# Performance work log

Measured on AMD Instinct MI355X. Metric: run time of the kernel, lower is better.

The kernel has to match this reference:

```python
import jax, jax.numpy as jnp
import numpy as np

TRANSLATE_STD = 0.125
SCALE_STD = 0.2
CUTOUT_SIZE = 0.5

B, C, H, W = 64, 3, 512, 512


def setup_inputs() -> dict:
    key = jax.random.key(0)
    ks = jax.random.split(key, 20)
    inp = {
        'images': jax.random.normal(ks[0], (B, C, H, W), dtype=jnp.float32),
        'u_angle': jax.random.uniform(ks[1], (B,), dtype=jnp.float32),
        'u_scale': jax.random.uniform(ks[2], (B,), dtype=jnp.float32),
        'u_trans': jax.random.uniform(ks[3], (B,), dtype=jnp.float32),
        'u_bright': jax.random.uniform(ks[4], (B,), dtype=jnp.float32),
        'u_contrast': jax.random.uniform(ks[5], (B,), dtype=jnp.float32),
        'u_sat': jax.random.uniform(ks[6], (B,), dtype=jnp.float32),
        'noise': jax.random.normal(ks[7], (B, C, H, W), dtype=jnp.float32),
        'm_flip': jax.random.randint(ks[8], (B,), 0, 2, dtype=jnp.int32),
        'm_rot': jax.random.randint(ks[9], (B,), 0, 2, dtype=jnp.int32),
        'm_scale': jax.random.randint(ks[10], (B,), 0, 2, dtype=jnp.int32),
        'm_trans': jax.random.randint(ks[11], (B,), 0, 2, dtype=jnp.int32),
        'm_bright': jax.random.randint(ks[12], (B,), 0, 2, dtype=jnp.int32),
        'm_contrast': jax.random.randint(ks[13], (B,), 0, 2, dtype=jnp.int32),
        'm_sat': jax.random.randint(ks[14], (B,), 0, 2, dtype=jnp.int32),
        'm_cut': jax.random.randint(ks[15], (B,), 0, 2, dtype=jnp.int32),
        'y0': jax.random.randint(ks[16], (B,), 0, H - int(H * CUTOUT_SIZE) + 1, dtype=jnp.int32),
        'x0': jax.random.randint(ks[17], (B,), 0, W - int(W * CUTOUT_SIZE) + 1, dtype=jnp.int32),
    }
    return inp


def _sample_bilinear_reflect(img, gx, gy):
    # img: [C,H,W]; gx, gy: [H,W] normalized coords in grid_sample convention
    # (align_corners=False, padding_mode='reflection')
    c, h, w = img.shape
    x = ((gx + 1.0) * w - 1.0) * 0.5
    y = ((gy + 1.0) * h - 1.0) * 0.5

    def reflect(v, size):
        # reflect about pixel edges [-0.5, size-0.5], then clip coordinate
        v = jnp.abs(v + 0.5)
        v = jnp.mod(v, 2.0 * size)
        v = jnp.minimum(v, 2.0 * size - v)
        return jnp.clip(v - 0.5, 0.0, size - 1.0)

    x = reflect(x, float(w))
    y = reflect(y, float(h))
    x0f = jnp.floor(x)
    y0f = jnp.floor(y)
    wx = x - x0f
    wy = y - y0f
    x0i = jnp.clip(x0f, 0, w - 1).astype(jnp.int32)
    x1i = jnp.clip(x0f + 1, 0, w - 1).astype(jnp.int32)
    y0i = jnp.clip(y0f, 0, h - 1).astype(jnp.int32)
    y1i = jnp.clip(y0f + 1, 0, h - 1).astype(jnp.int32)
    v00 = img[:, y0i, x0i]
    v01 = img[:, y0i, x1i]
    v10 = img[:, y1i, x0i]
    v11 = img[:, y1i, x1i]
    top = v00 + wx * (v01 - v00)
    bot = v10 + wx * (v11 - v10)
    return top + wy * (bot - top)


def reference(images, u_angle, u_scale, u_trans, u_bright, u_contrast, u_sat,
              noise, m_flip, m_rot, m_scale, m_trans, m_bright, m_contrast,
              m_sat, m_cut, y0, x0):
    b, c, h, w = images.shape
    # xflip
    images = jnp.where((m_flip > 0)[:, None, None, None], images[..., ::-1], images)
    # rotate / scale / translate (single value broadcast to both axes, as in original)
    angle = jnp.where(m_rot > 0, (u_angle * 2.0 - 1.0) * jnp.pi, 0.0)
    sc = jnp.where(m_scale > 0, (u_scale * 2.0 - 1.0) * SCALE_STD + 1.0, 1.0)
    tr = jnp.where(m_trans > 0, (u_trans * 2.0 - 1.0) * TRANSLATE_STD, 0.0)
    ca = jnp.cos(angle)[:, None, None]
    sa = jnp.sin(angle)[:, None, None]
    scb = sc[:, None, None]
    trb = tr[:, None, None]
    gx0, gy0 = jnp.meshgrid(jnp.linspace(-1.0, 1.0, w), jnp.linspace(-1.0, 1.0, h), indexing='xy')  # [H,W]
    gx = scb * (ca * gx0 - sa * gy0) + trb  # [B,H,W]
    gy = scb * (sa * gx0 + ca * gy0) + trb
    images = jax.vmap(_sample_bilinear_reflect)(images, gx, gy)
    # brightness
    bb = jnp.where(m_bright > 0, u_bright * 0.2, 0.0)
    images = jnp.clip(images + bb[:, None, None, None], -1.0, 1.0)
    # contrast
    cc = jnp.where(m_contrast > 0, u_contrast + 0.5, 1.0)
    images = jnp.clip(images * cc[:, None, None, None], -1.0, 1.0)
    # saturation: lerp(grayscale, images, s)
    ss = jnp.where(m_sat > 0, u_sat * 2.0, 1.0)[:, None, None, None]
    gray = images.mean(axis=1, keepdims=True)
    images = jnp.clip(gray + ss * (images - gray), -1.0, 1.0)
    ch, cw = int(h * CUTOUT_SIZE), int(w * CUTOUT_SIZE)
    ys = jnp.arange(h)[None, :, None]
    xs = jnp.arange(w)[None, None, :]
    y0b = y0[:, None, None]
    x0b = x0[:, None, None]
    cmask = (ys >= y0b) & (ys < y0b + ch) & (xs >= x0b) & (xs < x0b + cw)
    fmask = cmask & (m_cut > 0)[:, None, None]
    images = jnp.where(fmask[:, None, :, :], noise, images)
    return images
```

## Files before the change

### kernel.cpp

```cpp
#include <hip/hip_runtime.h>
#include <math.h>


constexpr int Bn = 64;
constexpr int Cn = 3;
constexpr int Hn = 512;
constexpr int Wn = 512;
constexpr float TRANSLATE_STD = 0.125f;
constexpr float SCALE_STD = 0.2f;
constexpr int CUT_H = 256;
constexpr int CUT_W = 256;

typedef float f2v __attribute__((ext_vector_type(2)));

__device__ __forceinline__ f2v load2(const float* p) {
    f2v r;
    __builtin_memcpy(&r, p, 8);
    return r;
}

__device__ __forceinline__ float reflect_coord(float v, float size) {
    v = fabsf(v + 0.5f);
    v = fmodf(v, 2.0f * size);
    v = fminf(v, 2.0f * size - v);
    return fminf(fmaxf(v - 0.5f, 0.0f), size - 1.0f);
}

__global__ __launch_bounds__(256) void augment_kernel(
    const float* __restrict__ images,
    const float* __restrict__ u_angle,
    const float* __restrict__ u_scale,
    const float* __restrict__ u_trans,
    const float* __restrict__ u_bright,
    const float* __restrict__ u_contrast,
    const float* __restrict__ u_sat,
    const float* __restrict__ noise,
    const int* __restrict__ m_flip,
    const int* __restrict__ m_rot,
    const int* __restrict__ m_scale,
    const int* __restrict__ m_trans,
    const int* __restrict__ m_bright,
    const int* __restrict__ m_contrast,
    const int* __restrict__ m_sat,
    const int* __restrict__ m_cut,
    const int* __restrict__ y0p,
    const int* __restrict__ x0p,
    float* __restrict__ out)
{
    const int x = blockIdx.x * 32 + threadIdx.x;
    const int y = blockIdx.y * 8 + threadIdx.y;
    const int b = blockIdx.z;

    const float angle = (m_rot[b] > 0) ? (u_angle[b] * 2.0f - 1.0f) * 3.14159265358979323846f : 0.0f;
    const float sc    = (m_scale[b] > 0) ? (u_scale[b] * 2.0f - 1.0f) * SCALE_STD + 1.0f : 1.0f;
    const float tr    = (m_trans[b] > 0) ? (u_trans[b] * 2.0f - 1.0f) * TRANSLATE_STD : 0.0f;
    const float bb    = (m_bright[b] > 0) ? u_bright[b] * 0.2f : 0.0f;
    const float cc    = (m_contrast[b] > 0) ? u_contrast[b] + 0.5f : 1.0f;
    const float ss    = (m_sat[b] > 0) ? u_sat[b] * 2.0f : 1.0f;
    const bool  flip  = m_flip[b] > 0;
    const bool  docut = m_cut[b] > 0;
    const int   cy0   = y0p[b];
    const int   cx0   = x0p[b];

    float saf, caf;
    __sincosf(angle, &saf, &caf);

    const float gx0 = -1.0f + (2.0f / 511.0f) * (float)x;
    const float gy0 = -1.0f + (2.0f / 511.0f) * (float)y;

    const float gx = sc * (caf * gx0 - saf * gy0) + tr;
    const float gy = sc * (saf * gx0 + caf * gy0) + tr;

    float xx = ((gx + 1.0f) * (float)Wn - 1.0f) * 0.5f;
    float yy = ((gy + 1.0f) * (float)Hn - 1.0f) * 0.5f;
    xx = reflect_coord(xx, (float)Wn);
    yy = reflect_coord(yy, (float)Hn);

    const float x0f = floorf(xx);
    const float y0f = floorf(yy);
    const float wx = xx - x0f;
    const float wy = yy - y0f;

    int x0i = (int)fminf(fmaxf(x0f, 0.0f), (float)(Wn - 1));
    int x1i = (int)fminf(x0f + 1.0f, (float)(Wn - 1));
    const int y0i = (int)fminf(fmaxf(y0f, 0.0f), (float)(Hn - 1));
    const int y1i = (int)fminf(y0f + 1.0f, (float)(Hn - 1));

    if (flip) { x0i = (Wn - 1) - x0i; x1i = (Wn - 1) - x1i; }

    const int xbase = min(min(x0i, x1i), Wn - 2);
    const bool s0 = (x0i != xbase);
    const bool s1 = (x1i != xbase);

    const size_t plane = (size_t)Hn * Wn;
    const float* imgb = images + (size_t)b * Cn * plane;
    const int r0 = y0i * Wn + xbase;
    const int r1 = y1i * Wn + xbase;

    float vals[Cn];
    #pragma unroll
    for (int c = 0; c < Cn; ++c) {
        const float* p = imgb + (size_t)c * plane;
        const f2v t0 = load2(p + r0);
        const f2v t1 = load2(p + r1);
        const float v00 = s0 ? t0.y : t0.x;
        const float v01 = s1 ? t0.y : t0.x;
        const float v10 = s0 ? t1.y : t1.x;
        const float v11 = s1 ? t1.y : t1.x;
        const float top = v00 + wx * (v01 - v00);
        const float bot = v10 + wx * (v11 - v10);
        float v = top + wy * (bot - top);
        v = fminf(fmaxf(v + bb, -1.0f), 1.0f);
        v = fminf(fmaxf(v * cc, -1.0f), 1.0f);
        vals[c] = v;
    }

    const float gray = (vals[0] + vals[1] + vals[2]) * (1.0f / 3.0f);
    const bool cut = docut && (y >= cy0) && (y < cy0 + CUT_H) && (x >= cx0) && (x < cx0 + CUT_W);

    const size_t base = (size_t)b * Cn * plane + (size_t)y * Wn + (size_t)x;
    #pragma unroll
    for (int c = 0; c < Cn; ++c) {
        float v = gray + ss * (vals[c] - gray);
        v = fminf(fmaxf(v, -1.0f), 1.0f);
        if (cut) v = __builtin_nontemporal_load(&noise[base + c * plane]);
        __builtin_nontemporal_store(v, &out[base + c * plane]);
    }
}

extern "C" void kernel_launch(void* const* d_in, const int* in_sizes, int n_in,
                              void* d_out, int out_size, void* d_ws, size_t ws_size,
                              hipStream_t stream) {
    const float* images     = (const float*)d_in[0];
    const float* u_angle    = (const float*)d_in[1];
    const float* u_scale    = (const float*)d_in[2];
    const float* u_trans    = (const float*)d_in[3];
    const float* u_bright   = (const float*)d_in[4];
    const float* u_contrast = (const float*)d_in[5];
    const float* u_sat      = (const float*)d_in[6];
    const float* noise      = (const float*)d_in[7];
    const int*   m_flip     = (const int*)d_in[8];
    const int*   m_rot      = (const int*)d_in[9];
    const int*   m_scale    = (const int*)d_in[10];
    const int*   m_trans    = (const int*)d_in[11];
    const int*   m_bright   = (const int*)d_in[12];
    const int*   m_contrast = (const int*)d_in[13];
    const int*   m_sat      = (const int*)d_in[14];
    const int*   m_cut      = (const int*)d_in[15];
    const int*   y0p        = (const int*)d_in[16];
    const int*   x0p        = (const int*)d_in[17];
    float* out = (float*)d_out;

    dim3 block(32, 8);
    dim3 grid(Wn / 32, Hn / 8, Bn);
    augment_kernel<<<grid, block, 0, stream>>>(
        images, u_angle, u_scale, u_trans, u_bright, u_contrast, u_sat, noise,
        m_flip, m_rot, m_scale, m_trans, m_bright, m_contrast, m_sat, m_cut,
        y0p, x0p, out);
}
```

Measured before the change: 511.4 us.

## Stage source footprint of each tile in LDS for bilinear gather

Each 32x8 block works out the bounding box its tile maps to in the source image by transforming the tile's four corners. When that box lies inside the image and fits in the LDS capacity, the block cooperatively copies the footprint for all three channels into shared memory, with flip applied. It then does the bilinear sampling from LDS instead of issuing scattered global gathers. Blocks whose footprint needs reflection or is too large fall back to the original global-gather path, and the staged path adds a __syncthreads plus about 15KB of LDS per block.

```diff
diff --git a/kernel.cpp b/kernel.cpp
--- a/kernel.cpp
+++ b/kernel.cpp
@@ -10,6 +10,8 @@
 constexpr float SCALE_STD = 0.2f;
 constexpr int CUT_H = 256;
 constexpr int CUT_W = 256;
+
+constexpr int LDS_CAP = 1280;
 
 typedef float f2v __attribute__((ext_vector_type(2)));
 
@@ -47,6 +49,8 @@
     const int* __restrict__ x0p,
     float* __restrict__ out)
 {
+    __shared__ float lds[Cn * LDS_CAP];
+
     const int x = blockIdx.x * 32 + threadIdx.x;
     const int y = blockIdx.y * 8 + threadIdx.y;
     const int b = blockIdx.z;
@@ -65,54 +69,141 @@
     float saf, caf;
     __sincosf(angle, &saf, &caf);
 
-    const float gx0 = -1.0f + (2.0f / 511.0f) * (float)x;
-    const float gy0 = -1.0f + (2.0f / 511.0f) * (float)y;
-
-    const float gx = sc * (caf * gx0 - saf * gy0) + tr;
-    const float gy = sc * (saf * gx0 + caf * gy0) + tr;
-
-    float xx = ((gx + 1.0f) * (float)Wn - 1.0f) * 0.5f;
-    float yy = ((gy + 1.0f) * (float)Hn - 1.0f) * 0.5f;
-    xx = reflect_coord(xx, (float)Wn);
-    yy = reflect_coord(yy, (float)Hn);
-
-    const float x0f = floorf(xx);
-    const float y0f = floorf(yy);
-    const float wx = xx - x0f;
-    const float wy = yy - y0f;
-
-    int x0i = (int)fminf(fmaxf(x0f, 0.0f), (float)(Wn - 1));
-    int x1i = (int)fminf(x0f + 1.0f, (float)(Wn - 1));
-    const int y0i = (int)fminf(fmaxf(y0f, 0.0f), (float)(Hn - 1));
-    const int y1i = (int)fminf(y0f + 1.0f, (float)(Hn - 1));
-
-    if (flip) { x0i = (Wn - 1) - x0i; x1i = (Wn - 1) - x1i; }
-
-    const int xbase = min(min(x0i, x1i), Wn - 2);
-    const bool s0 = (x0i != xbase);
-    const bool s1 = (x1i != xbase);
+    auto coord = [&](float fx, float fy, float& oxx, float& oyy) {
+        const float gx0 = -1.0f + (2.0f / 511.0f) * fx;
+        const float gy0 = -1.0f + (2.0f / 511.0f) * fy;
+        const float gx = sc * (caf * gx0 - saf * gy0) + tr;
+        const float gy = sc * (saf * gx0 + caf * gy0) + tr;
+        oxx = ((gx + 1.0f) * (float)Wn - 1.0f) * 0.5f;
+        oyy = ((gy + 1.0f) * (float)Hn - 1.0f) * 0.5f;
+    };
+
+    float xx, yy;
+    coord((float)x, (float)y, xx, yy);
+
+    const float tx0 = (float)(blockIdx.x * 32);
+    const float tx1 = tx0 + 31.0f;
+    const float ty0 = (float)(blockIdx.y * 8);
+    const float ty1 = ty0 + 7.0f;
+    float cxx0, cyy0, cxx1, cyy1, cxx2, cyy2, cxx3, cyy3;
+    coord(tx0, ty0, cxx0, cyy0);
+    coord(tx1, ty0, cxx1, cyy1);
+    coord(tx0, ty1, cxx2, cyy2);
+    coord(tx1, ty1, cxx3, cyy3);
+    const float minxx = fminf(fminf(cxx0, cxx1), fminf(cxx2, cxx3));
+    const float maxxx = fmaxf(fmaxf(cxx0, cxx1), fmaxf(cxx2, cxx3));
+    const float minyy = fminf(fminf(cyy0, cyy1), fminf(cyy2, cyy3));
+    const float maxyy = fmaxf(fmaxf(cyy0, cyy1), fmaxf(cyy2, cyy3));
+
+    bool staged = (minxx >= -0.9f) && (maxxx <= 511.9f) &&
+                  (minyy >= -0.9f) && (maxyy <= 511.9f);
+
+    int x_lo = 0, x_hi = 1, y_lo = 0, y_hi = 1, fw = 2, fh = 2;
+    if (staged) {
+        x_lo = max(0, (int)floorf(minxx));
+        x_hi = min(Wn - 1, (int)floorf(maxxx) + 1);
+        x_lo = max(0, min(x_lo, x_hi - 1));
+        y_lo = max(0, (int)floorf(minyy));
+        y_hi = min(Hn - 1, (int)floorf(maxyy) + 1);
+        y_lo = max(0, min(y_lo, y_hi - 1));
+        fw = x_hi - x_lo + 1;
+        fh = y_hi - y_lo + 1;
+        if (fw * fh > LDS_CAP) staged = false;
+    }
 
     const size_t plane = (size_t)Hn * Wn;
     const float* imgb = images + (size_t)b * Cn * plane;
-    const int r0 = y0i * Wn + xbase;
-    const int r1 = y1i * Wn + xbase;
 
     float vals[Cn];
-    #pragma unroll
-    for (int c = 0; c < Cn; ++c) {
-        const float* p = imgb + (size_t)c * plane;
-        const f2v t0 = load2(p + r0);
-        const f2v t1 = load2(p + r1);
-        const float v00 = s0 ? t0.y : t0.x;
-        const float v01 = s1 ? t0.y : t0.x;
-        const float v10 = s0 ? t1.y : t1.x;
-        const float v11 = s1 ? t1.y : t1.x;
-        const float top = v00 + wx * (v01 - v00);
-        const float bot = v10 + wx * (v11 - v10);
-        float v = top + wy * (bot - top);
-        v = fminf(fmaxf(v + bb, -1.0f), 1.0f);
-        v = fminf(fmaxf(v * cc, -1.0f), 1.0f);
-        vals[c] = v;
+
+    if (staged) {
+        #pragma unroll
+        for (int c = 0; c < Cn; ++c) {
+            const float* src = imgb + (size_t)c * plane;
+            float* dst = &lds[c * LDS_CAP];
+            for (int ry = threadIdx.y; ry < fh; ry += 8) {
+                const float* rowp = src + (size_t)(y_lo + ry) * Wn;
+                for (int rx = threadIdx.x; rx < fw; rx += 32) {
+                    const int gxc = x_lo + rx;
+                    dst[ry * fw + rx] = rowp[flip ? (Wn - 1 - gxc) : gxc];
+                }
+            }
+        }
+        __syncthreads();
+
+        const float x0f = floorf(xx);
+        const float y0f = floorf(yy);
+        const float wx = xx - x0f;
+        const float wy = yy - y0f;
+        const int x0i = (int)x0f;
+        const int y0i = (int)y0f;
+
+        const int xa = min(max(x0i, x_lo), x_hi);
+        const int xb = min(max(x0i + 1, x_lo), x_hi);
+        const int pb = min(xa, x_hi - 1);
+        const bool s0 = (xa != pb);
+        const bool s1 = (xb != pb);
+        const int ya = min(max(y0i, y_lo), y_hi) - y_lo;
+        const int yb = min(max(y0i + 1, y_lo), y_hi) - y_lo;
+        const int col = pb - x_lo;
+        const int off0 = ya * fw + col;
+        const int off1 = yb * fw + col;
+
+        #pragma unroll
+        for (int c = 0; c < Cn; ++c) {
+            const float* ch = &lds[c * LDS_CAP];
+            const float t0x = ch[off0], t0y = ch[off0 + 1];
+            const float t1x = ch[off1], t1y = ch[off1 + 1];
+            const float v00 = s0 ? t0y : t0x;
+            const float v01 = s1 ? t0y : t0x;
+            const float v10 = s0 ? t1y : t1x;
+            const float v11 = s1 ? t1y : t1x;
+            const float top = v00 + wx * (v01 - v00);
+            const float bot = v10 + wx * (v11 - v10);
+            float v = top + wy * (bot - top);
+            v = fminf(fmaxf(v + bb, -1.0f), 1.0f);
+            v = fminf(fmaxf(v * cc, -1.0f), 1.0f);
+            vals[c] = v;
+        }
+    } else {
+        const float rxx = reflect_coord(xx, (float)Wn);
+        const float ryy = reflect_coord(yy, (float)Hn);
+
+        const float x0f = floorf(rxx);
+        const float y0f = floorf(ryy);
+        const float wx = rxx - x0f;
+        const float wy = ryy - y0f;
+
+        int x0i = (int)fminf(fmaxf(x0f, 0.0f), (float)(Wn - 1));
+        int x1i = (int)fminf(x0f + 1.0f, (float)(Wn - 1));
+        const int y0i = (int)fminf(fmaxf(y0f, 0.0f), (float)(Hn - 1));
+        const int y1i = (int)fminf(y0f + 1.0f, (float)(Hn - 1));
+
+        if (flip) { x0i = (Wn - 1) - x0i; x1i = (Wn - 1) - x1i; }
+
+        const int xbase = min(min(x0i, x1i), Wn - 2);
+        const bool s0 = (x0i != xbase);
+        const bool s1 = (x1i != xbase);
+
+        const int r0 = y0i * Wn + xbase;
+        const int r1 = y1i * Wn + xbase;
+
+        #pragma unroll
+        for (int c = 0; c < Cn; ++c) {
+            const float* p = imgb + (size_t)c * plane;
+            const f2v t0 = load2(p + r0);
+            const f2v t1 = load2(p + r1);
+            const float v00 = s0 ? t0.y : t0.x;
+            const float v01 = s1 ? t0.y : t0.x;
+            const float v10 = s0 ? t1.y : t1.x;
+            const float v11 = s1 ? t1.y : t1.x;
+            const float top = v00 + wx * (v01 - v00);
+            const float bot = v10 + wx * (v11 - v10);
+            float v = top + wy * (bot - top);
+            v = fminf(fmaxf(v + bb, -1.0f), 1.0f);
+            v = fminf(fmaxf(v * cc, -1.0f), 1.0f);
+            vals[c] = v;
+        }
     }
 
     const float gray = (vals[0] + vals[1] + vals[2]) * (1.0f / 3.0f);
```

New measurement: 634.0 us. +24.0%, slower.

## Stage interior tile source footprints in LDS and swizzle blocks per XCD

Applied to the files above, without the earlier changes.

Switches to 16x16 tiles. For tiles whose rotated and scaled source footprint stays inside the image and fits in 32 rows, the block cooperatively loads that footprint for all three channels into shared memory, applying the flip during the load, and then does the bilinear taps from LDS. Edge tiles fall back to the original per-pixel global gather with reflection. The block index is also remapped so that contiguous tile ranges land on the same XCD, aiming for better L2 locality. This cuts redundant scattered global loads, at the cost of a barrier, extra staging work and the assumption that the footprint width stays within 32 columns.

```diff
diff --git a/kernel.cpp b/kernel.cpp
--- a/kernel.cpp
+++ b/kernel.cpp
@@ -10,6 +10,11 @@
 constexpr float SCALE_STD = 0.2f;
 constexpr int CUT_H = 256;
 constexpr int CUT_W = 256;
+
+constexpr int FW = 32;
+constexpr int FSTRIDE = 40;
+constexpr int FH_MAX = 32;
+constexpr int CH_LDS = FSTRIDE * FH_MAX;
 
 typedef float f2v __attribute__((ext_vector_type(2)));
 
@@ -47,9 +52,16 @@
     const int* __restrict__ x0p,
     float* __restrict__ out)
 {
-    const int x = blockIdx.x * 32 + threadIdx.x;
-    const int y = blockIdx.y * 8 + threadIdx.y;
-    const int b = blockIdx.z;
+    __shared__ __align__(16) float lds[Cn * CH_LDS];
+
+    const int lin = blockIdx.x + (blockIdx.y << 5) + (blockIdx.z << 10);
+    const int swz = ((lin & 7) << 13) + (lin >> 3);
+    const int tx16 = (swz & 31) << 4;
+    const int ty16 = ((swz >> 5) & 31) << 4;
+    const int b    = swz >> 10;
+
+    const int x = tx16 + threadIdx.x;
+    const int y = ty16 + threadIdx.y;
 
     const float angle = (m_rot[b] > 0) ? (u_angle[b] * 2.0f - 1.0f) * 3.14159265358979323846f : 0.0f;
     const float sc    = (m_scale[b] > 0) ? (u_scale[b] * 2.0f - 1.0f) * SCALE_STD + 1.0f : 1.0f;
@@ -65,54 +77,150 @@
     float saf, caf;
     __sincosf(angle, &saf, &caf);
 
-    const float gx0 = -1.0f + (2.0f / 511.0f) * (float)x;
-    const float gy0 = -1.0f + (2.0f / 511.0f) * (float)y;
-
-    const float gx = sc * (caf * gx0 - saf * gy0) + tr;
-    const float gy = sc * (saf * gx0 + caf * gy0) + tr;
-
-    float xx = ((gx + 1.0f) * (float)Wn - 1.0f) * 0.5f;
-    float yy = ((gy + 1.0f) * (float)Hn - 1.0f) * 0.5f;
-    xx = reflect_coord(xx, (float)Wn);
-    yy = reflect_coord(yy, (float)Hn);
-
-    const float x0f = floorf(xx);
-    const float y0f = floorf(yy);
-    const float wx = xx - x0f;
-    const float wy = yy - y0f;
-
-    int x0i = (int)fminf(fmaxf(x0f, 0.0f), (float)(Wn - 1));
-    int x1i = (int)fminf(x0f + 1.0f, (float)(Wn - 1));
-    const int y0i = (int)fminf(fmaxf(y0f, 0.0f), (float)(Hn - 1));
-    const int y1i = (int)fminf(y0f + 1.0f, (float)(Hn - 1));
-
-    if (flip) { x0i = (Wn - 1) - x0i; x1i = (Wn - 1) - x1i; }
-
-    const int xbase = min(min(x0i, x1i), Wn - 2);
-    const bool s0 = (x0i != xbase);
-    const bool s1 = (x1i != xbase);
+    auto coord = [&](float fx, float fy, float& oxx, float& oyy) {
+        const float gx0 = -1.0f + (2.0f / 511.0f) * fx;
+        const float gy0 = -1.0f + (2.0f / 511.0f) * fy;
+        const float gx = sc * (caf * gx0 - saf * gy0) + tr;
+        const float gy = sc * (saf * gx0 + caf * gy0) + tr;
+        oxx = ((gx + 1.0f) * (float)Wn - 1.0f) * 0.5f;
+        oyy = ((gy + 1.0f) * (float)Hn - 1.0f) * 0.5f;
+    };
+
+    float xx, yy;
+    coord((float)x, (float)y, xx, yy);
+
+    float xx00, yy00;
+    coord((float)tx16, (float)ty16, xx00, yy00);
+    const float k  = sc * (512.0f / 511.0f);
+    const float px = caf * k * 15.0f;
+    const float qx = -saf * k * 15.0f;
+    const float py = saf * k * 15.0f;
+    const float qy = caf * k * 15.0f;
+    const float minxx = xx00 + fminf(px, 0.0f) + fminf(qx, 0.0f);
+    const float maxxx = xx00 + fmaxf(px, 0.0f) + fmaxf(qx, 0.0f);
+    const float minyy = yy00 + fminf(py, 0.0f) + fminf(qy, 0.0f);
+    const float maxyy = yy00 + fmaxf(py, 0.0f) + fmaxf(qy, 0.0f);
+
+    bool interior = (minxx >= 1.0f) && (maxxx <= 509.0f) &&
+                    (minyy >= 1.0f) && (maxyy <= 509.0f);
+
+    int x_lo = 0, y_lo = 0, fh = 0;
+    if (interior) {
+        x_lo = min((int)minxx - 1, Wn - FW);
+        y_lo = (int)minyy - 1;
+        fh = ((int)maxyy + 2) - y_lo + 1;
+        if (fh > FH_MAX) interior = false;
+    }
 
     const size_t plane = (size_t)Hn * Wn;
     const float* imgb = images + (size_t)b * Cn * plane;
-    const int r0 = y0i * Wn + xbase;
-    const int r1 = y1i * Wn + xbase;
 
     float vals[Cn];
-    #pragma unroll
-    for (int c = 0; c < Cn; ++c) {
-        const float* p = imgb + (size_t)c * plane;
-        const f2v t0 = load2(p + r0);
-        const f2v t1 = load2(p + r1);
-        const float v00 = s0 ? t0.y : t0.x;
-        const float v01 = s1 ? t0.y : t0.x;
-        const float v10 = s0 ? t1.y : t1.x;
-        const float v11 = s1 ? t1.y : t1.x;
-        const float top = v00 + wx * (v01 - v00);
-        const float bot = v10 + wx * (v11 - v10);
-        float v = top + wy * (bot - top);
-        v = fminf(fmaxf(v + bb, -1.0f), 1.0f);
-        v = fminf(fmaxf(v * cc, -1.0f), 1.0f);
-        vals[c] = v;
+
+    if (interior) {
+        const int tid = threadIdx.y * 16 + threadIdx.x;
+        const int k2  = (tid & 15) * 2;
+        const int sry = tid >> 4;
+        const int scol = flip ? (Wn - 2 - (x_lo + k2)) : (x_lo + k2);
+        const float* sp = imgb + (size_t)(y_lo + sry) * Wn + scol;
+        const bool p1 = sry < fh;
+        const bool p2 = sry + 16 < fh;
+
+        f2v va0{}, vb0{}, vc0{}, va1{}, vb1{}, vc1{};
+        if (p1) {
+            va0 = load2(sp);
+            vb0 = load2(sp + plane);
+            vc0 = load2(sp + 2 * plane);
+        }
+        if (p2) {
+            const float* sp2 = sp + 16 * Wn;
+            va1 = load2(sp2);
+            vb1 = load2(sp2 + plane);
+            vc1 = load2(sp2 + 2 * plane);
+        }
+        if (flip) {
+            f2v t;
+            t = va0; va0.x = t.y; va0.y = t.x;
+            t = vb0; vb0.x = t.y; vb0.y = t.x;
+            t = vc0; vc0.x = t.y; vc0.y = t.x;
+            t = va1; va1.x = t.y; va1.y = t.x;
+            t = vb1; vb1.x = t.y; vb1.y = t.x;
+            t = vc1; vc1.x = t.y; vc1.y = t.x;
+        }
+        float* dst = &lds[sry * FSTRIDE + k2];
+        if (p1) {
+            *(f2v*)(dst)              = va0;
+            *(f2v*)(dst + CH_LDS)     = vb0;
+            *(f2v*)(dst + 2 * CH_LDS) = vc0;
+        }
+        if (p2) {
+            *(f2v*)(dst + 16 * FSTRIDE)              = va1;
+            *(f2v*)(dst + CH_LDS + 16 * FSTRIDE)     = vb1;
+            *(f2v*)(dst + 2 * CH_LDS + 16 * FSTRIDE) = vc1;
+        }
+        __syncthreads();
+
+        const float fx = xx - (float)x_lo;
+        const float fy = yy - (float)y_lo;
+        const int xi = (int)fx;
+        const int yi = (int)fy;
+        const float wx = fx - (float)xi;
+        const float wy = fy - (float)yi;
+        const float* ph = &lds[yi * FSTRIDE + xi];
+
+        #pragma unroll
+        for (int c = 0; c < Cn; ++c) {
+            const float v00 = ph[0];
+            const float v01 = ph[1];
+            const float v10 = ph[FSTRIDE];
+            const float v11 = ph[FSTRIDE + 1];
+            ph += CH_LDS;
+            const float top = v00 + wx * (v01 - v00);
+            const float bot = v10 + wx * (v11 - v10);
+            float v = top + wy * (bot - top);
+            v = fminf(fmaxf(v + bb, -1.0f), 1.0f);
+            v = fminf(fmaxf(v * cc, -1.0f), 1.0f);
+            vals[c] = v;
+        }
+    } else {
+        const float rxx = reflect_coord(xx, (float)Wn);
+        const float ryy = reflect_coord(yy, (float)Hn);
+
+        const float x0f = floorf(rxx);
+        const float y0f = floorf(ryy);
+        const float wx = rxx - x0f;
+        const float wy = ryy - y0f;
+
+        int x0i = (int)fminf(fmaxf(x0f, 0.0f), (float)(Wn - 1));
+        int x1i = (int)fminf(x0f + 1.0f, (float)(Wn - 1));
+        const int y0i = (int)fminf(fmaxf(y0f, 0.0f), (float)(Hn - 1));
+        const int y1i = (int)fminf(y0f + 1.0f, (float)(Hn - 1));
+
+        if (flip) { x0i = (Wn - 1) - x0i; x1i = (Wn - 1) - x1i; }
+
+        const int xbase = min(min(x0i, x1i), Wn - 2);
+        const bool s0 = (x0i != xbase);
+        const bool s1 = (x1i != xbase);
+
+        const int r0 = y0i * Wn + xbase;
+        const int r1 = y1i * Wn + xbase;
+
+        #pragma unroll
+        for (int c = 0; c < Cn; ++c) {
+            const float* p = imgb + (size_t)c * plane;
+            const f2v t0 = load2(p + r0);
+            const f2v t1 = load2(p + r1);
+            const float v00 = s0 ? t0.y : t0.x;
+            const float v01 = s1 ? t0.y : t0.x;
+            const float v10 = s0 ? t1.y : t1.x;
+            const float v11 = s1 ? t1.y : t1.x;
+            const float top = v00 + wx * (v01 - v00);
+            const float bot = v10 + wx * (v11 - v10);
+            float v = top + wy * (bot - top);
+            v = fminf(fmaxf(v + bb, -1.0f), 1.0f);
+            v = fminf(fmaxf(v * cc, -1.0f), 1.0f);
+            vals[c] = v;
+        }
     }
 
     const float gray = (vals[0] + vals[1] + vals[2]) * (1.0f / 3.0f);
@@ -151,8 +259,8 @@
     const int*   x0p        = (const int*)d_in[17];
     float* out = (float*)d_out;
 
-    dim3 block(32, 8);
-    dim3 grid(Wn / 32, Hn / 8, Bn);
+    dim3 block(16, 16);
+    dim3 grid(Wn / 16, Hn / 16, Bn);
     augment_kernel<<<grid, block, 0, stream>>>(
         images, u_angle, u_scale, u_trans, u_bright, u_contrast, u_sat, noise,
         m_flip, m_rot, m_scale, m_trans, m_bright, m_contrast, m_sat, m_cut,
```

Result: no change. 507.9 us (-0.7%).

## Stage source footprints in double-buffered LDS and sweep tiles per block row

Applied to the files above, without the earlier changes.

Each block now handles a 16-row strip of one image and walks across it in 16x16 tiles. For each tile it computes the bounding box of the rotated source footprint, loads that box cooperatively into a double-buffered LDS tile, and prefetches the next tile's box while the current one is sampled. Tiles whose footprint touches the border or exceeds the LDS height fall back to direct global gathers with reflection. The goal is to replace scattered uncoalesced gathers with coalesced loads and LDS reuse. The cost is barriers per tile, extra LDS pressure and more complex code. The grid is also remapped with a batch and row swizzle.

```diff
diff --git a/kernel.cpp b/kernel.cpp
--- a/kernel.cpp
+++ b/kernel.cpp
@@ -11,6 +11,13 @@
 constexpr int CUT_H = 256;
 constexpr int CUT_W = 256;
 
+constexpr int FW = 32;
+constexpr int FSTRIDE = 41;
+constexpr int FH_MAX = 32;
+constexpr int CH_LDS = FSTRIDE * FH_MAX;
+constexpr int BUF_LDS = Cn * CH_LDS;
+constexpr int NT = 32;
+
 typedef float f2v __attribute__((ext_vector_type(2)));
 
 __device__ __forceinline__ f2v load2(const float* p) {
@@ -24,6 +31,12 @@
     v = fmodf(v, 2.0f * size);
     v = fminf(v, 2.0f * size - v);
     return fminf(fmaxf(v - 0.5f, 0.0f), size - 1.0f);
+}
+
+__device__ __forceinline__ void pipe_barrier() {
+    asm volatile("s_waitcnt lgkmcnt(0)" ::: "memory");
+    __builtin_amdgcn_s_barrier();
+    __builtin_amdgcn_sched_barrier(0);
 }
 
 __global__ __launch_bounds__(256) void augment_kernel(
@@ -47,9 +60,17 @@
     const int* __restrict__ x0p,
     float* __restrict__ out)
 {
-    const int x = blockIdx.x * 32 + threadIdx.x;
-    const int y = blockIdx.y * 8 + threadIdx.y;
-    const int b = blockIdx.z;
+    __shared__ __align__(16) float lds[2 * BUF_LDS];
+
+    const int bid = blockIdx.x;
+    const int jj  = bid >> 3;
+    const int lb  = jj >> 5;
+    const int b   = (bid & 7) * 8 + lb;
+    const int trow = ((jj & 31) + lb * 13) & 31;
+
+    const int tx  = threadIdx.x;
+    const int tyy = threadIdx.y;
+    const int y   = trow * 16 + tyy;
 
     const float angle = (m_rot[b] > 0) ? (u_angle[b] * 2.0f - 1.0f) * 3.14159265358979323846f : 0.0f;
     const float sc    = (m_scale[b] > 0) ? (u_scale[b] * 2.0f - 1.0f) * SCALE_STD + 1.0f : 1.0f;
@@ -65,66 +86,195 @@
     float saf, caf;
     __sincosf(angle, &saf, &caf);
 
-    const float gx0 = -1.0f + (2.0f / 511.0f) * (float)x;
-    const float gy0 = -1.0f + (2.0f / 511.0f) * (float)y;
-
-    const float gx = sc * (caf * gx0 - saf * gy0) + tr;
-    const float gy = sc * (saf * gx0 + caf * gy0) + tr;
-
-    float xx = ((gx + 1.0f) * (float)Wn - 1.0f) * 0.5f;
-    float yy = ((gy + 1.0f) * (float)Hn - 1.0f) * 0.5f;
-    xx = reflect_coord(xx, (float)Wn);
-    yy = reflect_coord(yy, (float)Hn);
-
-    const float x0f = floorf(xx);
-    const float y0f = floorf(yy);
-    const float wx = xx - x0f;
-    const float wy = yy - y0f;
-
-    int x0i = (int)fminf(fmaxf(x0f, 0.0f), (float)(Wn - 1));
-    int x1i = (int)fminf(x0f + 1.0f, (float)(Wn - 1));
-    const int y0i = (int)fminf(fmaxf(y0f, 0.0f), (float)(Hn - 1));
-    const int y1i = (int)fminf(y0f + 1.0f, (float)(Hn - 1));
-
-    if (flip) { x0i = (Wn - 1) - x0i; x1i = (Wn - 1) - x1i; }
-
-    const int xbase = min(min(x0i, x1i), Wn - 2);
-    const bool s0 = (x0i != xbase);
-    const bool s1 = (x1i != xbase);
+    const float kk = sc * (512.0f / 511.0f);
+    const float dxdx = caf * kk, dxdy = -saf * kk;
+    const float dydx = saf * kk, dydy = caf * kk;
+    const float xx_org = 256.0f * (sc * (saf - caf) + tr + 1.0f) - 0.5f;
+    const float yy_org = 256.0f * (sc * (-saf - caf) + tr + 1.0f) - 0.5f;
+
+    const float tstep_x = 16.0f * dxdx;
+    const float tstep_y = 16.0f * dydx;
+
+    float xxt = xx_org + (float)tx * dxdx + (float)y * dxdy;
+    float yyt = yy_org + (float)tx * dydx + (float)y * dydy;
+
+    const float fty = (float)(trow * 16);
+    const float bx0 = xx_org + fty * dxdy;
+    const float by0 = yy_org + fty * dydy;
+    const float sxx = 15.0f * dxdx, sxy = 15.0f * dxdy;
+    const float syx = 15.0f * dydx, syy = 15.0f * dydy;
+    const float min_dx = fminf(sxx, 0.0f) + fminf(sxy, 0.0f);
+    const float max_dx = fmaxf(sxx, 0.0f) + fmaxf(sxy, 0.0f);
+    const float min_dy = fminf(syx, 0.0f) + fminf(syy, 0.0f);
+    const float max_dy = fmaxf(syx, 0.0f) + fmaxf(syy, 0.0f);
 
     const size_t plane = (size_t)Hn * Wn;
     const float* imgb = images + (size_t)b * Cn * plane;
-    const int r0 = y0i * Wn + xbase;
-    const int r1 = y1i * Wn + xbase;
-
-    float vals[Cn];
-    #pragma unroll
-    for (int c = 0; c < Cn; ++c) {
-        const float* p = imgb + (size_t)c * plane;
-        const f2v t0 = load2(p + r0);
-        const f2v t1 = load2(p + r1);
-        const float v00 = s0 ? t0.y : t0.x;
-        const float v01 = s1 ? t0.y : t0.x;
-        const float v10 = s0 ? t1.y : t1.x;
-        const float v11 = s1 ? t1.y : t1.x;
-        const float top = v00 + wx * (v01 - v00);
-        const float bot = v10 + wx * (v11 - v10);
-        float v = top + wy * (bot - top);
-        v = fminf(fmaxf(v + bb, -1.0f), 1.0f);
-        v = fminf(fmaxf(v * cc, -1.0f), 1.0f);
-        vals[c] = v;
-    }
-
-    const float gray = (vals[0] + vals[1] + vals[2]) * (1.0f / 3.0f);
-    const bool cut = docut && (y >= cy0) && (y < cy0 + CUT_H) && (x >= cx0) && (x < cx0 + CUT_W);
-
-    const size_t base = (size_t)b * Cn * plane + (size_t)y * Wn + (size_t)x;
-    #pragma unroll
-    for (int c = 0; c < Cn; ++c) {
-        float v = gray + ss * (vals[c] - gray);
-        v = fminf(fmaxf(v, -1.0f), 1.0f);
-        if (cut) v = __builtin_nontemporal_load(&noise[base + c * plane]);
-        __builtin_nontemporal_store(v, &out[base + c * plane]);
+
+    const int tid = tyy * 16 + tx;
+    const int k2  = (tid & 15) * 2;
+    const int sry = tid >> 4;
+    const size_t srow = (size_t)sry * Wn;
+
+    const bool ycut = docut && (y >= cy0) && (y < cy0 + CUT_H);
+    const size_t obase = (size_t)b * Cn * plane + (size_t)y * Wn;
+
+    auto mkbox = [&](float bxt, float byt, int& x_lo, int& y_lo, int& fh, bool& ok) {
+        const float minxx = bxt + min_dx, maxxx = bxt + max_dx;
+        const float minyy = byt + min_dy, maxyy = byt + max_dy;
+        ok = (minxx >= 1.0f) && (maxxx <= 509.0f) &&
+             (minyy >= 1.0f) && (maxyy <= 509.0f);
+        x_lo = 0; y_lo = 0; fh = 0;
+        if (ok) {
+            x_lo = min((int)minxx - 1, Wn - FW);
+            y_lo = (int)minyy - 1;
+            fh   = ((int)maxyy + 2) - y_lo + 1;
+            if (fh > FH_MAX) ok = false;
+        }
+    };
+
+    f2v a0{}, b0{}, c0{}, a1{}, b1{}, c1{};
+
+    auto issueR = [&](int x_lo, int y_lo, int fh) {
+        const int scol = flip ? (Wn - 2 - (x_lo + k2)) : (x_lo + k2);
+        const float* sp = imgb + (size_t)y_lo * Wn + srow + scol;
+        if (sry < fh) {
+            a0 = load2(sp);
+            b0 = load2(sp + plane);
+            c0 = load2(sp + 2 * plane);
+        }
+        if (sry + 16 < fh) {
+            const float* sp2 = sp + 16 * Wn;
+            a1 = load2(sp2);
+            b1 = load2(sp2 + plane);
+            c1 = load2(sp2 + 2 * plane);
+        }
+    };
+
+    auto writeR = [&](float* buf, int fh) {
+        float* d = buf + sry * FSTRIDE + k2;
+        if (sry < fh) {
+            if (flip) {
+                d[0] = a0.y; d[1] = a0.x;
+                d[CH_LDS] = b0.y; d[CH_LDS + 1] = b0.x;
+                d[2 * CH_LDS] = c0.y; d[2 * CH_LDS + 1] = c0.x;
+            } else {
+                d[0] = a0.x; d[1] = a0.y;
+                d[CH_LDS] = b0.x; d[CH_LDS + 1] = b0.y;
+                d[2 * CH_LDS] = c0.x; d[2 * CH_LDS + 1] = c0.y;
+            }
+        }
+        if (sry + 16 < fh) {
+            float* d2 = d + 16 * FSTRIDE;
+            if (flip) {
+                d2[0] = a1.y; d2[1] = a1.x;
+                d2[CH_LDS] = b1.y; d2[CH_LDS + 1] = b1.x;
+                d2[2 * CH_LDS] = c1.y; d2[2 * CH_LDS + 1] = c1.x;
+            } else {
+                d2[0] = a1.x; d2[1] = a1.y;
+                d2[CH_LDS] = b1.x; d2[CH_LDS + 1] = b1.y;
+                d2[2 * CH_LDS] = c1.x; d2[2 * CH_LDS + 1] = c1.y;
+            }
+        }
+    };
+
+    int cx_lo, cy_lo, cfh; bool cok;
+    int nx_lo, ny_lo, nfh; bool nok;
+
+    mkbox(bx0, by0, cx_lo, cy_lo, cfh, cok);
+    if (cok) { issueR(cx_lo, cy_lo, cfh); writeR(lds, cfh); }
+    mkbox(bx0 + tstep_x, by0 + tstep_y, nx_lo, ny_lo, nfh, nok);
+    if (nok) issueR(nx_lo, ny_lo, nfh);
+    float bxn = bx0 + 2.0f * tstep_x;
+    float byn = by0 + 2.0f * tstep_y;
+    pipe_barrier();
+
+    #pragma unroll 1
+    for (int t = 0; t < NT; ++t) {
+        float vals[Cn];
+
+        if (cok) {
+            const float* buf = lds + (t & 1) * BUF_LDS;
+            const float fx = xxt - (float)cx_lo;
+            const float fy = yyt - (float)cy_lo;
+            const int xi = (int)fx;
+            const int yi = (int)fy;
+            const float wx = fx - (float)xi;
+            const float wy = fy - (float)yi;
+            const float* ph = buf + yi * FSTRIDE + xi;
+            #pragma unroll
+            for (int c = 0; c < Cn; ++c) {
+                const float v00 = ph[0], v01 = ph[1];
+                const float v10 = ph[FSTRIDE], v11 = ph[FSTRIDE + 1];
+                ph += CH_LDS;
+                const float top = v00 + wx * (v01 - v00);
+                const float bot = v10 + wx * (v11 - v10);
+                float v = top + wy * (bot - top);
+                v = fminf(fmaxf(v + bb, -1.0f), 1.0f);
+                v = fminf(fmaxf(v * cc, -1.0f), 1.0f);
+                vals[c] = v;
+            }
+        } else {
+            const float rxx = reflect_coord(xxt, (float)Wn);
+            const float ryy = reflect_coord(yyt, (float)Hn);
+            const float x0f = floorf(rxx);
+            const float y0f = floorf(ryy);
+            const float wx = rxx - x0f;
+            const float wy = ryy - y0f;
+            int x0i = (int)fminf(fmaxf(x0f, 0.0f), (float)(Wn - 1));
+            int x1i = (int)fminf(x0f + 1.0f, (float)(Wn - 1));
+            const int y0i = (int)fminf(fmaxf(y0f, 0.0f), (float)(Hn - 1));
+            const int y1i = (int)fminf(y0f + 1.0f, (float)(Hn - 1));
+            if (flip) { x0i = (Wn - 1) - x0i; x1i = (Wn - 1) - x1i; }
+            const int xbase = min(min(x0i, x1i), Wn - 2);
+            const bool s0 = (x0i != xbase);
+            const bool s1 = (x1i != xbase);
+            const int r0 = y0i * Wn + xbase;
+            const int r1 = y1i * Wn + xbase;
+            #pragma unroll
+            for (int c = 0; c < Cn; ++c) {
+                const float* p = imgb + (size_t)c * plane;
+                const f2v t0 = load2(p + r0);
+                const f2v t1 = load2(p + r1);
+                const float v00 = s0 ? t0.y : t0.x;
+                const float v01 = s1 ? t0.y : t0.x;
+                const float v10 = s0 ? t1.y : t1.x;
+                const float v11 = s1 ? t1.y : t1.x;
+                const float top = v00 + wx * (v01 - v00);
+                const float bot = v10 + wx * (v11 - v10);
+                float v = top + wy * (bot - top);
+                v = fminf(fmaxf(v + bb, -1.0f), 1.0f);
+                v = fminf(fmaxf(v * cc, -1.0f), 1.0f);
+                vals[c] = v;
+            }
+        }
+
+        const int x = (t << 4) + tx;
+        const float gray = (vals[0] + vals[1] + vals[2]) * (1.0f / 3.0f);
+        const bool cut = ycut && (x >= cx0) && (x < cx0 + CUT_W);
+        const size_t base = obase + (size_t)x;
+        #pragma unroll
+        for (int c = 0; c < Cn; ++c) {
+            float v = gray + ss * (vals[c] - gray);
+            v = fminf(fmaxf(v, -1.0f), 1.0f);
+            if (cut) v = __builtin_nontemporal_load(&noise[base + c * plane]);
+            __builtin_nontemporal_store(v, &out[base + c * plane]);
+        }
+
+        float* wbuf = lds + ((t & 1) ^ 1) * BUF_LDS;
+        if (nok) writeR(wbuf, nfh);
+
+        cx_lo = nx_lo; cy_lo = ny_lo; cfh = nfh; cok = nok;
+        if (t + 2 < NT) {
+            mkbox(bxn, byn, nx_lo, ny_lo, nfh, nok);
+            if (nok) issueR(nx_lo, ny_lo, nfh);
+        } else {
+            nok = false;
+        }
+        bxn += tstep_x; byn += tstep_y;
+        xxt += tstep_x; yyt += tstep_y;
+
+        pipe_barrier();
     }
 }
 
@@ -151,8 +301,8 @@
     const int*   x0p        = (const int*)d_in[17];
     float* out = (float*)d_out;
 
-    dim3 block(32, 8);
-    dim3 grid(Wn / 32, Hn / 8, Bn);
+    dim3 block(16, 16);
+    dim3 grid(Bn * 32, 1, 1);
     augment_kernel<<<grid, block, 0, stream>>>(
         images, u_angle, u_scale, u_trans, u_bright, u_contrast, u_sat, noise,
         m_flip, m_rot, m_scale, m_trans, m_bright, m_contrast, m_sat, m_cut,
```

Result: slower. 551.6 us (+7.9%).
